# Optimization experiments

Measured on AMD Instinct MI355X. Metric: run time of the kernel, lower is better.

Reference implementation:

```python
import jax, jax.numpy as jnp
import numpy as np

N = 10000      # nodes
E = 160000     # edges
D = 512        # hidden = input channels (residual requires equality)
OUT = 128      # output channels
G = 64         # graphs in batch


def setup_inputs() -> dict:
    key = jax.random.key(0)
    ks = jax.random.split(key, 16)
    s = 1.0 / np.sqrt(D)
    inp = {
        "x": jax.random.normal(ks[0], (N, D), jnp.float32) * 0.1,
        "edge_index": jax.random.randint(ks[1], (2, E), 0, N, dtype=jnp.int64),
        "batch": jnp.sort(jax.random.randint(ks[2], (N,), 0, G, dtype=jnp.int64)),
    }
    for i in range(5):
        inp[f"Wr{i+1}"] = jax.random.uniform(ks[3 + 2 * i], (D, D), jnp.float32, -s, s)  # lin_rel weight
        inp[f"Ws{i+1}"] = jax.random.uniform(ks[4 + 2 * i], (D, D), jnp.float32, -s, s)  # lin_root weight (no bias)
        inp[f"b{i+1}"] = jnp.zeros((D,), jnp.float32)                                     # lin_rel bias
    inp["Wlin"] = jax.random.uniform(ks[13], (D, OUT), jnp.float32, -s, s)
    inp["blin"] = jnp.zeros((OUT,), jnp.float32)
    return inp


def graph_conv(x, src, dst, Wr, Ws, b):
    # PyG GraphConv(aggr='add'): out = lin_rel(sum_{j in N(i)} x_j) + lin_root(x_i)
    agg = jax.ops.segment_sum(x[src], dst, num_segments=N)  # [N, D] scatter-add
    return agg @ Wr + b + x @ Ws


def reference(x, Wr1, Ws1, b1, Wr2, Ws2, b2, Wr3, Ws3, b3, Wr4, Ws4, b4, Wr5, Ws5, b5, Wlin, blin, edge_index, batch):
    src, dst = edge_index[0], edge_index[1]
    x = jax.nn.relu(x + graph_conv(x, src, dst, Wr1, Ws1, b1))
    x = jax.nn.relu(x + graph_conv(x, src, dst, Wr2, Ws2, b2))
    x = jax.nn.relu(x + graph_conv(x, src, dst, Wr3, Ws3, b3))
    x = jax.nn.relu(x + graph_conv(x, src, dst, Wr4, Ws4, b4))
    x = x + graph_conv(x, src, dst, Wr5, Ws5, b5)  # no relu after conv5
    # global_mean_pool over graph ids
    sums = jax.ops.segment_sum(x, batch, num_segments=G)                       # [G, D]
    cnt = jax.ops.segment_sum(jnp.ones((N, 1), x.dtype), batch, num_segments=G)
    x = sums / jnp.maximum(cnt, 1.0)
    return x @ Wlin + blin  # [G, OUT]
```

## Files before the change

### kernel.cpp

```cpp
#include <hip/hip_runtime.h>
#include <hip/hip_bf16.h>

#define NN 10000
#define EE 160000
#define DD 512
#define GG 64
#define OUTC 128
#define NBLK 628

typedef __attribute__((ext_vector_type(8))) short bf16x8;
typedef __attribute__((ext_vector_type(4))) float f32x4;

static __device__ __forceinline__ unsigned short f2bf(float f) {
  unsigned u = __builtin_bit_cast(unsigned, f);
  unsigned rounding = 0x7fffu + ((u >> 16) & 1u);
  u += rounding;
  return (unsigned short)(u >> 16);
}

static __device__ __forceinline__ void gload_lds16(const void* g, void* l) {
  __builtin_amdgcn_global_load_lds(
      (const __attribute__((address_space(1))) unsigned*)g,
      (__attribute__((address_space(3))) unsigned*)l, 16, 0, 0);
}

__global__ void hist_dst(const int* __restrict__ dst, int* __restrict__ cnt) {
  int e = blockIdx.x * 256 + threadIdx.x;
  if (e < EE) atomicAdd(&cnt[dst[e]], 1);
}

__global__ void scan_offsets(const int* __restrict__ cnt, int* __restrict__ offs) {
  __shared__ int wpre[17];
  __shared__ int carry;
  int t = threadIdx.x;
  int lane = t & 63, wv = t >> 6;
  if (t == 0) carry = 0;
  __syncthreads();
  for (int base = 0; base < NN; base += 1024) {
    int i = base + t;
    int v = (i < NN) ? cnt[i] : 0;
    int s = v;
#pragma unroll
    for (int d = 1; d < 64; d <<= 1) {
      int o = __shfl_up(s, d, 64);
      if (lane >= d) s += o;
    }
    if (lane == 63) wpre[wv] = s;
    __syncthreads();
    if (t == 0) {
      int r = 0;
      for (int w = 0; w < 16; ++w) { int x = wpre[w]; wpre[w] = r; r += x; }
      wpre[16] = r;
    }
    __syncthreads();
    int incl = s + wpre[wv] + carry;
    if (i < NN) offs[i] = incl - v;
    __syncthreads();
    if (t == 0) carry += wpre[16];
    __syncthreads();
  }
  if (t == 0) offs[NN] = carry;
}

__global__ void fill_edges(const int* __restrict__ src, const int* __restrict__ dst,
                           const int* __restrict__ offs, int* __restrict__ fptr,
                           int* __restrict__ ssrc) {
  int e = blockIdx.x * 256 + threadIdx.x;
  if (e < EE) {
    int d = dst[e];
    int p = atomicAdd(&fptr[d], 1);
    ssrc[offs[d] + p] = src[e];
  }
}

struct WPtrs { const float* p[10]; };

__global__ void transpose_w_all(WPtrs wp, unsigned short* __restrict__ WT) {
  __shared__ float tile[32][33];
  int z = blockIdx.z;
  const float* W = wp.p[z];
  unsigned short* dst = WT + (size_t)(z >> 1) * DD * 1024 + (size_t)(z & 1) * DD;
  int bx = blockIdx.x * 32, by = blockIdx.y * 32;
  int tx = threadIdx.x, ty = threadIdx.y;
  for (int i = ty; i < 32; i += 8)
    tile[i][tx] = W[(size_t)(by + i) * DD + bx + tx];
  __syncthreads();
  int addI = z & 1;
  for (int i = ty; i < 32; i += 8) {
    float v = tile[tx][i];
    if (addI && (by + tx) == (bx + i)) v += 1.0f;
    dst[(size_t)(bx + i) * 1024 + by + tx] = f2bf(v);
  }
}

__global__ void convert_x(const float* __restrict__ x, unsigned short* __restrict__ m0) {
  int i = blockIdx.x * 256 + threadIdx.x;
  if (i < NN * DD / 2) {
    float2 v = ((const float2*)x)[i];
    unsigned u = (unsigned)f2bf(v.x) | ((unsigned)f2bf(v.y) << 16);
    int e = i << 1;
    int row = e >> 9, col = e & 511;
    ((unsigned*)m0)[row * 512 + 256 + (col >> 1)] = u;
  }
}

__global__ __launch_bounds__(256) void seg_sum_sliced(unsigned short* __restrict__ merged,
                                                      const int* __restrict__ offs,
                                                      const int* __restrict__ ssrc) {
  int bid = blockIdx.x;
  int s8 = bid & 7;
  int g = bid >> 3;
  int slice = s8 & 3, sub = s8 >> 2;
  int wave = threadIdx.x >> 6, lane = threadIdx.x & 63;
  int node = (sub * 1250 + g) * 4 + wave;
  int beg = offs[node], end = offs[node + 1];
  const unsigned* xw = (const unsigned*)merged;
  int co = 256 + slice * 64 + lane;
  float a0 = 0.f, a1 = 0.f;
  int e = beg;
#define SEG_LD(i) unsigned v##i = xw[(size_t)ssrc[e + i] * 512 + co]
#define SEG_AC(i)                                          \
  a0 += __builtin_bit_cast(float, v##i << 16);             \
  a1 += __builtin_bit_cast(float, v##i & 0xffff0000u)
  for (; e + 8 <= end; e += 8) {
    SEG_LD(0); SEG_LD(1); SEG_LD(2); SEG_LD(3);
    SEG_LD(4); SEG_LD(5); SEG_LD(6); SEG_LD(7);
    SEG_AC(0); SEG_AC(1); SEG_AC(2); SEG_AC(3);
    SEG_AC(4); SEG_AC(5); SEG_AC(6); SEG_AC(7);
  }
  for (; e + 4 <= end; e += 4) {
    SEG_LD(0); SEG_LD(1); SEG_LD(2); SEG_LD(3);
    SEG_AC(0); SEG_AC(1); SEG_AC(2); SEG_AC(3);
  }
  for (; e < end; ++e) {
    unsigned v = xw[(size_t)ssrc[e] * 512 + co];
    a0 += __builtin_bit_cast(float, v << 16);
    a1 += __builtin_bit_cast(float, v & 0xffff0000u);
  }
#undef SEG_LD
#undef SEG_AC
  unsigned o = (unsigned)f2bf(a0) | ((unsigned)f2bf(a1) << 16);
  ((unsigned*)merged)[(size_t)node * 512 + slice * 64 + lane] = o;
}

__global__ __launch_bounds__(256) void gemm_layer(
    const unsigned short* __restrict__ Am,
    const unsigned short* __restrict__ Bw,
    const float* __restrict__ bias,
    unsigned short* __restrict__ xout,
    int do_relu) {
  __shared__ unsigned short Al[2][64 * 64];
  __shared__ unsigned short Bl[2][128 * 64];
  int tid = threadIdx.x;
  int lane = tid & 63, wave = tid >> 6;
  int wr = wave >> 1, wc = wave & 1;

  int orig = blockIdx.x;
  int xcd = orig & 7, cidx = orig >> 3;
  int wgid = (xcd < 4) ? xcd * 79 + cidx : 316 + (xcd - 4) * 78 + cidx;
  int brow = (wgid >> 2) * 64;
  int bcol = (wgid & 3) * 128;
  int lrow = lane & 15, lq = lane >> 4;

  f32x4 acc[2][4];
#pragma unroll
  for (int m = 0; m < 2; ++m)
#pragma unroll
    for (int n = 0; n < 4; ++n) acc[m][n] = (f32x4){0.f, 0.f, 0.f, 0.f};

  auto STAGE = [&](int buf, int t) {
    int k0 = t * 64;
#pragma unroll
    for (int i = 0; i < 2; ++i) {
      int idx = i * 256 + tid;
      int row = idx >> 3, c = idx & 7;
      int csw = (c ^ (row & 7)) * 8;
      int gr = brow + row;
      if (gr >= NN) gr = NN - 1;
      gload_lds16(Am + (size_t)gr * 1024 + k0 + csw, &Al[buf][idx * 8]);
    }
#pragma unroll
    for (int i = 0; i < 4; ++i) {
      int idx = i * 256 + tid;
      int row = idx >> 3, c = idx & 7;
      int csw = (c ^ (row & 7)) * 8;
      gload_lds16(Bw + (size_t)(bcol + row) * 1024 + k0 + csw, &Bl[buf][idx * 8]);
    }
  };

  STAGE(0, 0);
  __syncthreads();
  int cur = 0;
#pragma unroll 1
  for (int t = 0; t < 16; ++t) {
    if (t < 15) STAGE(cur ^ 1, t + 1);
#pragma unroll
    for (int kk = 0; kk < 2; ++kk) {
      bf16x8 a[2], b[4];
      int lc = kk * 4 + lq;
#pragma unroll
      for (int m = 0; m < 2; ++m) {
        int row = wr * 32 + m * 16 + lrow;
        a[m] = *(const bf16x8*)&Al[cur][row * 64 + ((lc ^ (lrow & 7)) * 8)];
      }
#pragma unroll
      for (int n = 0; n < 4; ++n) {
        int row = wc * 64 + n * 16 + lrow;
        b[n] = *(const bf16x8*)&Bl[cur][row * 64 + ((lc ^ (lrow & 7)) * 8)];
      }
#pragma unroll
      for (int m = 0; m < 2; ++m)
#pragma unroll
        for (int n = 0; n < 4; ++n)
          acc[m][n] = __builtin_amdgcn_mfma_f32_16x16x32_bf16(a[m], b[n], acc[m][n], 0, 0, 0);
    }
    __syncthreads();
    cur ^= 1;
  }

  int crow = lq * 4, ccol = lrow;
#pragma unroll
  for (int m = 0; m < 2; ++m) {
#pragma unroll
    for (int n = 0; n < 4; ++n) {
      int col = bcol + wc * 64 + n * 16 + ccol;
      float bv = bias[col];
#pragma unroll
      for (int i = 0; i < 4; ++i) {
        int row = brow + wr * 32 + m * 16 + crow + i;
        if (row < NN) {
          float v = acc[m][n][i] + bv;
          if (do_relu) v = fmaxf(v, 0.f);
          xout[(size_t)row * 1024 + 512 + col] = f2bf(v);
        }
      }
    }
  }
}

__global__ void graph_bounds(const int* __restrict__ batch, int* __restrict__ gstart) {
  int i = blockIdx.x * 256 + threadIdx.x;
  if (i >= NN) return;
  int cur = batch[i];
  int prev = (i == 0) ? -1 : batch[i - 1];
  for (int g = prev + 1; g <= cur; ++g) gstart[g] = i;
  if (i == NN - 1)
    for (int g = cur + 1; g <= GG; ++g) gstart[g] = NN;
}

__global__ __launch_bounds__(256) void pool_partial(const unsigned short* __restrict__ mfin,
                                                    const int* __restrict__ gstart,
                                                    float* __restrict__ pooled) {
  int g = blockIdx.x, part = blockIdx.y;
  int t = threadIdx.x;
  int beg = gstart[g], end = gstart[g + 1];
  int n = end - beg;
  int per = (n + 7) >> 3;
  int b = beg + part * per;
  int e = b + per; if (e > end) e = end;
  if (b >= e) return;
  const unsigned* mw = (const unsigned*)mfin;
  float a0 = 0.f, a1 = 0.f;
  for (int r = b; r < e; ++r) {
    unsigned v = mw[(size_t)r * 512 + 256 + t];
    a0 += __builtin_bit_cast(float, v << 16);
    a1 += __builtin_bit_cast(float, v & 0xffff0000u);
  }
  atomicAdd(&pooled[g * DD + 2 * t], a0);
  atomicAdd(&pooled[g * DD + 2 * t + 1], a1);
}

__global__ __launch_bounds__(128) void final_linear(const float* __restrict__ pooled,
                                                    const int* __restrict__ gstart,
                                                    const float* __restrict__ Wlin,
                                                    const float* __restrict__ blin,
                                                    float* __restrict__ out) {
  __shared__ float p[128];
  int g = blockIdx.x, kq = blockIdx.y;
  int o = threadIdx.x;
  int cnt = gstart[g + 1] - gstart[g];
  float inv = 1.0f / fmaxf((float)cnt, 1.0f);
  p[o] = pooled[g * DD + kq * 128 + o] * inv;
  __syncthreads();
  float s = (kq == 0) ? blin[o] : 0.f;
#pragma unroll 8
  for (int k = 0; k < 128; ++k)
    s += p[k] * Wlin[(size_t)(kq * 128 + k) * OUTC + o];
  atomicAdd(&out[g * OUTC + o], s);
}

extern "C" void kernel_launch(void* const* d_in, const int* in_sizes, int n_in,
                              void* d_out, int out_size, void* d_ws, size_t ws_size,
                              hipStream_t stream) {
  const float* x_in = (const float*)d_in[0];
  const int* ei = (const int*)d_in[1];
  const int* src = ei;
  const int* dst = ei + EE;
  const int* batch = (const int*)d_in[2];
  WPtrs wp;
  const float* bias[5];
  for (int l = 0; l < 5; ++l) {
    wp.p[2 * l] = (const float*)d_in[3 + 3 * l];
    wp.p[2 * l + 1] = (const float*)d_in[4 + 3 * l];
    bias[l] = (const float*)d_in[5 + 3 * l];
  }
  const float* Wlin = (const float*)d_in[18];
  const float* blin = (const float*)d_in[19];
  float* out = (float*)d_out;

  char* ws = (char*)d_ws;
  size_t off = 0;
  auto alloc = [&](size_t bytes) { size_t o = off; off += (bytes + 511) & ~(size_t)511; return o; };
  unsigned short* m0 = (unsigned short*)(ws + alloc((size_t)NN * 1024 * 2));
  unsigned short* m1 = (unsigned short*)(ws + alloc((size_t)NN * 1024 * 2));
  unsigned short* wt = (unsigned short*)(ws + alloc((size_t)5 * DD * 1024 * 2));
  int* deg = (int*)(ws + alloc((size_t)2 * NN * 4));
  int* fptr = deg + NN;
  int* offs = (int*)(ws + alloc((size_t)(NN + 1) * 4));
  int* ssrc = (int*)(ws + alloc((size_t)EE * 4));
  int* gstart = (int*)(ws + alloc((size_t)(GG + 1) * 4));
  float* pooled = (float*)(ws + alloc((size_t)GG * DD * 4));

  hipMemsetAsync(deg, 0, (size_t)2 * NN * 4, stream);
  hipMemsetAsync(pooled, 0, (size_t)GG * DD * 4, stream);
  hipMemsetAsync(out, 0, (size_t)GG * OUTC * 4, stream);

  int eblocks = (EE + 255) / 256;
  hist_dst<<<eblocks, 256, 0, stream>>>(dst, deg);
  scan_offsets<<<1, 1024, 0, stream>>>(deg, offs);
  fill_edges<<<eblocks, 256, 0, stream>>>(src, dst, offs, fptr, ssrc);

  dim3 tb(32, 8), tg(DD / 32, DD / 32, 10);
  transpose_w_all<<<tg, tb, 0, stream>>>(wp, wt);

  convert_x<<<(NN * DD / 2 + 255) / 256, 256, 0, stream>>>(x_in, m0);

  graph_bounds<<<(NN + 255) / 256, 256, 0, stream>>>(batch, gstart);

  unsigned short* mc = m0;
  unsigned short* mn = m1;
  for (int l = 0; l < 5; ++l) {
    seg_sum_sliced<<<10000, 256, 0, stream>>>(mc, offs, ssrc);
    gemm_layer<<<NBLK, 256, 0, stream>>>(mc, wt + (size_t)l * DD * 1024,
                                         bias[l], mn, l < 4 ? 1 : 0);
    unsigned short* t = mc; mc = mn; mn = t;
  }

  dim3 pgrid(GG, 8);
  pool_partial<<<pgrid, 256, 0, stream>>>(mc, gstart, pooled);
  dim3 fgrid(GG, 4);
  final_linear<<<fgrid, 128, 0, stream>>>(pooled, gstart, Wlin, blin, out);
}
```

Measured before the change: 266.8 us.

## Merge prep kernels, pair nodes in segment sum, shrink GEMM tiles to 64x64

Four preprocessing kernels (weight transpose, x conversion, graph bounds, degree histogram) become one launch that branches on block index. The segment-sum kernel now has each wave gather two nodes at once, which keeps more independent loads in flight and halves the block count. The GEMM tile shrinks from 64x128 to 64x64, doubling the grid to 1256 blocks for better CU occupancy. The cost is less B-tile reuse per block and a simpler XCD remap.

```diff
diff --git a/kernel.cpp b/kernel.cpp
--- a/kernel.cpp
+++ b/kernel.cpp
@@ -6,7 +6,7 @@
 #define DD 512
 #define GG 64
 #define OUTC 128
-#define NBLK 628
+#define NBLK2 1256
 
 typedef __attribute__((ext_vector_type(8))) short bf16x8;
 typedef __attribute__((ext_vector_type(4))) float f32x4;
@@ -24,9 +24,54 @@
       (__attribute__((address_space(3))) unsigned*)l, 16, 0, 0);
 }
 
-__global__ void hist_dst(const int* __restrict__ dst, int* __restrict__ cnt) {
-  int e = blockIdx.x * 256 + threadIdx.x;
-  if (e < EE) atomicAdd(&cnt[dst[e]], 1);
+struct WPtrs { const float* p[10]; };
+
+__global__ __launch_bounds__(256) void prep_all(
+    WPtrs wp, unsigned short* __restrict__ WT,
+    const float* __restrict__ x_in, unsigned short* __restrict__ m0,
+    const int* __restrict__ batch, int* __restrict__ gstart,
+    const int* __restrict__ dstv, int* __restrict__ deg) {
+  int bid = blockIdx.x;
+  int tid = threadIdx.x;
+  if (bid < 2560) {
+    __shared__ float tile[32][33];
+    int z = bid >> 8;
+    int rem = bid & 255;
+    int by = (rem >> 4) * 32, bx = (rem & 15) * 32;
+    const float* W = wp.p[z];
+    unsigned short* dst = WT + (size_t)(z >> 1) * DD * 1024 + (size_t)(z & 1) * DD;
+    int tx = tid & 31, ty = tid >> 5;
+    for (int i = ty; i < 32; i += 8)
+      tile[i][tx] = W[(size_t)(by + i) * DD + bx + tx];
+    __syncthreads();
+    int addI = z & 1;
+    for (int i = ty; i < 32; i += 8) {
+      float v = tile[tx][i];
+      if (addI && (by + tx) == (bx + i)) v += 1.0f;
+      dst[(size_t)(bx + i) * 1024 + by + tx] = f2bf(v);
+    }
+  } else if (bid < 12560) {
+    int i = (bid - 2560) * 256 + tid;
+    if (i < NN * DD / 2) {
+      float2 v = ((const float2*)x_in)[i];
+      unsigned u = (unsigned)f2bf(v.x) | ((unsigned)f2bf(v.y) << 16);
+      int e = i << 1;
+      int row = e >> 9, col = e & 511;
+      ((unsigned*)m0)[row * 512 + 256 + (col >> 1)] = u;
+    }
+  } else if (bid < 12600) {
+    int i = (bid - 12560) * 256 + tid;
+    if (i < NN) {
+      int cur = batch[i];
+      int prev = (i == 0) ? -1 : batch[i - 1];
+      for (int g = prev + 1; g <= cur; ++g) gstart[g] = i;
+      if (i == NN - 1)
+        for (int g = cur + 1; g <= GG; ++g) gstart[g] = NN;
+    }
+  } else {
+    int e = (bid - 12600) * 256 + tid;
+    if (e < EE) atomicAdd(&deg[dstv[e]], 1);
+  }
 }
 
 __global__ void scan_offsets(const int* __restrict__ cnt, int* __restrict__ offs) {
@@ -73,74 +118,55 @@
   }
 }
 
-struct WPtrs { const float* p[10]; };
-
-__global__ void transpose_w_all(WPtrs wp, unsigned short* __restrict__ WT) {
-  __shared__ float tile[32][33];
-  int z = blockIdx.z;
-  const float* W = wp.p[z];
-  unsigned short* dst = WT + (size_t)(z >> 1) * DD * 1024 + (size_t)(z & 1) * DD;
-  int bx = blockIdx.x * 32, by = blockIdx.y * 32;
-  int tx = threadIdx.x, ty = threadIdx.y;
-  for (int i = ty; i < 32; i += 8)
-    tile[i][tx] = W[(size_t)(by + i) * DD + bx + tx];
-  __syncthreads();
-  int addI = z & 1;
-  for (int i = ty; i < 32; i += 8) {
-    float v = tile[tx][i];
-    if (addI && (by + tx) == (bx + i)) v += 1.0f;
-    dst[(size_t)(bx + i) * 1024 + by + tx] = f2bf(v);
-  }
-}
-
-__global__ void convert_x(const float* __restrict__ x, unsigned short* __restrict__ m0) {
-  int i = blockIdx.x * 256 + threadIdx.x;
-  if (i < NN * DD / 2) {
-    float2 v = ((const float2*)x)[i];
-    unsigned u = (unsigned)f2bf(v.x) | ((unsigned)f2bf(v.y) << 16);
-    int e = i << 1;
-    int row = e >> 9, col = e & 511;
-    ((unsigned*)m0)[row * 512 + 256 + (col >> 1)] = u;
-  }
-}
-
-__global__ __launch_bounds__(256) void seg_sum_sliced(unsigned short* __restrict__ merged,
-                                                      const int* __restrict__ offs,
-                                                      const int* __restrict__ ssrc) {
+__global__ __launch_bounds__(256) void seg_sum2(unsigned short* __restrict__ merged,
+                                                const int* __restrict__ offs,
+                                                const int* __restrict__ ssrc) {
   int bid = blockIdx.x;
-  int s8 = bid & 7;
-  int g = bid >> 3;
-  int slice = s8 & 3, sub = s8 >> 2;
+  int slice = bid & 3;
+  int p = bid >> 2;
   int wave = threadIdx.x >> 6, lane = threadIdx.x & 63;
-  int node = (sub * 1250 + g) * 4 + wave;
-  int beg = offs[node], end = offs[node + 1];
+  int na = p * 4 + wave;
+  int nb = na + 5000;
   const unsigned* xw = (const unsigned*)merged;
-  int co = 256 + slice * 64 + lane;
-  float a0 = 0.f, a1 = 0.f;
-  int e = beg;
-#define SEG_LD(i) unsigned v##i = xw[(size_t)ssrc[e + i] * 512 + co]
-#define SEG_AC(i)                                          \
-  a0 += __builtin_bit_cast(float, v##i << 16);             \
-  a1 += __builtin_bit_cast(float, v##i & 0xffff0000u)
-  for (; e + 8 <= end; e += 8) {
-    SEG_LD(0); SEG_LD(1); SEG_LD(2); SEG_LD(3);
-    SEG_LD(4); SEG_LD(5); SEG_LD(6); SEG_LD(7);
-    SEG_AC(0); SEG_AC(1); SEG_AC(2); SEG_AC(3);
-    SEG_AC(4); SEG_AC(5); SEG_AC(6); SEG_AC(7);
-  }
-  for (; e + 4 <= end; e += 4) {
-    SEG_LD(0); SEG_LD(1); SEG_LD(2); SEG_LD(3);
-    SEG_AC(0); SEG_AC(1); SEG_AC(2); SEG_AC(3);
-  }
-  for (; e < end; ++e) {
-    unsigned v = xw[(size_t)ssrc[e] * 512 + co];
-    a0 += __builtin_bit_cast(float, v << 16);
-    a1 += __builtin_bit_cast(float, v & 0xffff0000u);
-  }
-#undef SEG_LD
-#undef SEG_AC
-  unsigned o = (unsigned)f2bf(a0) | ((unsigned)f2bf(a1) << 16);
-  ((unsigned*)merged)[(size_t)node * 512 + slice * 64 + lane] = o;
+  size_t co = 256 + slice * 64 + lane;
+  int e0 = offs[na], f0 = offs[na + 1];
+  int e1 = offs[nb], f1 = offs[nb + 1];
+  float a0 = 0.f, a1 = 0.f, b0 = 0.f, b1 = 0.f;
+#define LD(n, ee, i) unsigned n = xw[(size_t)ssrc[(ee) + (i)] * 512 + co]
+#define AC(n, x0, x1)                                   \
+  x0 += __builtin_bit_cast(float, n << 16);             \
+  x1 += __builtin_bit_cast(float, n & 0xffff0000u)
+  while (e0 + 8 <= f0 && e1 + 8 <= f1) {
+    LD(u0, e0, 0); LD(u1, e0, 1); LD(u2, e0, 2); LD(u3, e0, 3);
+    LD(u4, e0, 4); LD(u5, e0, 5); LD(u6, e0, 6); LD(u7, e0, 7);
+    LD(w0, e1, 0); LD(w1, e1, 1); LD(w2, e1, 2); LD(w3, e1, 3);
+    LD(w4, e1, 4); LD(w5, e1, 5); LD(w6, e1, 6); LD(w7, e1, 7);
+    AC(u0, a0, a1); AC(u1, a0, a1); AC(u2, a0, a1); AC(u3, a0, a1);
+    AC(u4, a0, a1); AC(u5, a0, a1); AC(u6, a0, a1); AC(u7, a0, a1);
+    AC(w0, b0, b1); AC(w1, b0, b1); AC(w2, b0, b1); AC(w3, b0, b1);
+    AC(w4, b0, b1); AC(w5, b0, b1); AC(w6, b0, b1); AC(w7, b0, b1);
+    e0 += 8; e1 += 8;
+  }
+  for (; e0 + 4 <= f0; e0 += 4) {
+    LD(u0, e0, 0); LD(u1, e0, 1); LD(u2, e0, 2); LD(u3, e0, 3);
+    AC(u0, a0, a1); AC(u1, a0, a1); AC(u2, a0, a1); AC(u3, a0, a1);
+  }
+  for (; e0 < f0; ++e0) {
+    LD(u0, e0, 0); AC(u0, a0, a1);
+  }
+  for (; e1 + 4 <= f1; e1 += 4) {
+    LD(w0, e1, 0); LD(w1, e1, 1); LD(w2, e1, 2); LD(w3, e1, 3);
+    AC(w0, b0, b1); AC(w1, b0, b1); AC(w2, b0, b1); AC(w3, b0, b1);
+  }
+  for (; e1 < f1; ++e1) {
+    LD(w0, e1, 0); AC(w0, b0, b1);
+  }
+#undef LD
+#undef AC
+  unsigned oa = (unsigned)f2bf(a0) | ((unsigned)f2bf(a1) << 16);
+  unsigned ob = (unsigned)f2bf(b0) | ((unsigned)f2bf(b1) << 16);
+  ((unsigned*)merged)[(size_t)na * 512 + slice * 64 + lane] = oa;
+  ((unsigned*)merged)[(size_t)nb * 512 + slice * 64 + lane] = ob;
 }
 
 __global__ __launch_bounds__(256) void gemm_layer(
@@ -150,23 +176,22 @@
     unsigned short* __restrict__ xout,
     int do_relu) {
   __shared__ unsigned short Al[2][64 * 64];
-  __shared__ unsigned short Bl[2][128 * 64];
+  __shared__ unsigned short Bl[2][64 * 64];
   int tid = threadIdx.x;
   int lane = tid & 63, wave = tid >> 6;
   int wr = wave >> 1, wc = wave & 1;
 
   int orig = blockIdx.x;
-  int xcd = orig & 7, cidx = orig >> 3;
-  int wgid = (xcd < 4) ? xcd * 79 + cidx : 316 + (xcd - 4) * 78 + cidx;
-  int brow = (wgid >> 2) * 64;
-  int bcol = (wgid & 3) * 128;
+  int wgid = (orig & 7) * 157 + (orig >> 3);
+  int brow = (wgid >> 3) * 64;
+  int bcol = (wgid & 7) * 64;
   int lrow = lane & 15, lq = lane >> 4;
 
-  f32x4 acc[2][4];
+  f32x4 acc[2][2];
 #pragma unroll
   for (int m = 0; m < 2; ++m)
 #pragma unroll
-    for (int n = 0; n < 4; ++n) acc[m][n] = (f32x4){0.f, 0.f, 0.f, 0.f};
+    for (int n = 0; n < 2; ++n) acc[m][n] = (f32x4){0.f, 0.f, 0.f, 0.f};
 
   auto STAGE = [&](int buf, int t) {
     int k0 = t * 64;
@@ -180,7 +205,7 @@
       gload_lds16(Am + (size_t)gr * 1024 + k0 + csw, &Al[buf][idx * 8]);
     }
 #pragma unroll
-    for (int i = 0; i < 4; ++i) {
+    for (int i = 0; i < 2; ++i) {
       int idx = i * 256 + tid;
       int row = idx >> 3, c = idx & 7;
       int csw = (c ^ (row & 7)) * 8;
@@ -196,7 +221,7 @@
     if (t < 15) STAGE(cur ^ 1, t + 1);
 #pragma unroll
     for (int kk = 0; kk < 2; ++kk) {
-      bf16x8 a[2], b[4];
+      bf16x8 a[2], b[2];
       int lc = kk * 4 + lq;
 #pragma unroll
       for (int m = 0; m < 2; ++m) {
@@ -204,14 +229,14 @@
         a[m] = *(const bf16x8*)&Al[cur][row * 64 + ((lc ^ (lrow & 7)) * 8)];
       }
 #pragma unroll
-      for (int n = 0; n < 4; ++n) {
-        int row = wc * 64 + n * 16 + lrow;
+      for (int n = 0; n < 2; ++n) {
+        int row = wc * 32 + n * 16 + lrow;
         b[n] = *(const bf16x8*)&Bl[cur][row * 64 + ((lc ^ (lrow & 7)) * 8)];
       }
 #pragma unroll
       for (int m = 0; m < 2; ++m)
 #pragma unroll
-        for (int n = 0; n < 4; ++n)
+        for (int n = 0; n < 2; ++n)
           acc[m][n] = __builtin_amdgcn_mfma_f32_16x16x32_bf16(a[m], b[n], acc[m][n], 0, 0, 0);
     }
     __syncthreads();
@@ -222,8 +247,8 @@
 #pragma unroll
   for (int m = 0; m < 2; ++m) {
 #pragma unroll
-    for (int n = 0; n < 4; ++n) {
-      int col = bcol + wc * 64 + n * 16 + ccol;
+    for (int n = 0; n < 2; ++n) {
+      int col = bcol + wc * 32 + n * 16 + ccol;
       float bv = bias[col];
 #pragma unroll
       for (int i = 0; i < 4; ++i) {
@@ -236,16 +261,6 @@
       }
     }
   }
-}
-
-__global__ void graph_bounds(const int* __restrict__ batch, int* __restrict__ gstart) {
-  int i = blockIdx.x * 256 + threadIdx.x;
-  if (i >= NN) return;
-  int cur = batch[i];
-  int prev = (i == 0) ? -1 : batch[i - 1];
-  for (int g = prev + 1; g <= cur; ++g) gstart[g] = i;
-  if (i == NN - 1)
-    for (int g = cur + 1; g <= GG; ++g) gstart[g] = NN;
 }
 
 __global__ __launch_bounds__(256) void pool_partial(const unsigned short* __restrict__ mfin,
@@ -325,24 +340,17 @@
   hipMemsetAsync(pooled, 0, (size_t)GG * DD * 4, stream);
   hipMemsetAsync(out, 0, (size_t)GG * OUTC * 4, stream);
 
-  int eblocks = (EE + 255) / 256;
-  hist_dst<<<eblocks, 256, 0, stream>>>(dst, deg);
+  prep_all<<<13225, 256, 0, stream>>>(wp, wt, x_in, m0, batch, gstart, dst, deg);
+
   scan_offsets<<<1, 1024, 0, stream>>>(deg, offs);
-  fill_edges<<<eblocks, 256, 0, stream>>>(src, dst, offs, fptr, ssrc);
-
-  dim3 tb(32, 8), tg(DD / 32, DD / 32, 10);
-  transpose_w_all<<<tg, tb, 0, stream>>>(wp, wt);
-
-  convert_x<<<(NN * DD / 2 + 255) / 256, 256, 0, stream>>>(x_in, m0);
-
-  graph_bounds<<<(NN + 255) / 256, 256, 0, stream>>>(batch, gstart);
+  fill_edges<<<(EE + 255) / 256, 256, 0, stream>>>(src, dst, offs, fptr, ssrc);
 
   unsigned short* mc = m0;
   unsigned short* mn = m1;
   for (int l = 0; l < 5; ++l) {
-    seg_sum_sliced<<<10000, 256, 0, stream>>>(mc, offs, ssrc);
-    gemm_layer<<<NBLK, 256, 0, stream>>>(mc, wt + (size_t)l * DD * 1024,
-                                         bias[l], mn, l < 4 ? 1 : 0);
+    seg_sum2<<<5000, 256, 0, stream>>>(mc, offs, ssrc);
+    gemm_layer<<<NBLK2, 256, 0, stream>>>(mc, wt + (size_t)l * DD * 1024,
+                                          bias[l], mn, l < 4 ? 1 : 0);
     unsigned short* t = mc; mc = mn; mn = t;
   }
 
```

Measured after the change: 289.2 us. 1.08x slower.
